# Optimization experiments

Hardware: AMD Instinct MI355X
Metric: run time of the kernel (lower is better)

Reference implementation:

```python
import math
import jax, jax.numpy as jnp
import numpy as np

H = 8
DIM = 256
HD = DIM // H
SCALE = math.sqrt(HD)
EPS = 1e-16


def _segment_softmax(scores, dst, num_nodes):
    # scores: [E, H], dst: [E] -> softmax over edges sharing the same dst
    m = jax.ops.segment_max(scores, dst, num_segments=num_nodes)  # [N, H]
    m = jnp.where(jnp.isfinite(m), m, 0.0)  # empty segments -> -inf -> 0
    e = jnp.exp(scores - m[dst])
    s = jax.ops.segment_sum(e, dst, num_segments=num_nodes)  # [N, H]
    return e / (s[dst] + EPS)


def _graph_attention(x, edges, wq, bq, wk, bk, wv, bv, wo, bo):
    # x: [N, DIM]; edges: [2, E] (src, dst). Dropout is identity (eval mode).
    N = x.shape[0]
    Q = (x @ wq + bq).reshape(N, H, HD)
    K = (x @ wk + bk).reshape(N, H, HD)
    V = (x @ wv + bv).reshape(N, H, HD)
    src, dst = edges[0], edges[1]
    scores = jnp.einsum('ehd,ehd->eh', Q[dst], K[src]) / SCALE  # [E, H]
    attn = _segment_softmax(scores, dst, N)  # [E, H]
    msgs = V[src] * attn[:, :, None]  # [E, H, HD]
    out = jax.ops.segment_sum(msgs, dst, num_segments=N).reshape(N, DIM)
    return out @ wo + bo


def _linear_params(key, fan_in, fan_out):
    k1, k2 = jax.random.split(key)
    bound = 1.0 / math.sqrt(fan_in)
    w = jax.random.uniform(k1, (fan_in, fan_out), minval=-bound, maxval=bound, dtype=jnp.float32)
    b = jax.random.uniform(k2, (fan_out,), minval=-bound, maxval=bound, dtype=jnp.float32)
    return w, b


def setup_inputs() -> dict:
    key = jax.random.key(0)
    ks = jax.random.split(key, 12)
    n_slot, n_dom = 20000, 1000
    e_slot, e_dom = 320000, 16000
    inp = {
        'slot_x': jax.random.normal(ks[0], (n_slot, DIM), dtype=jnp.float32),
        'domain_x': jax.random.normal(ks[1], (n_dom, DIM), dtype=jnp.float32),
        'slot_edges': jax.random.randint(ks[2], (2, e_slot), 0, n_slot, dtype=jnp.int32),
        'domain_edges': jax.random.randint(ks[3], (2, e_dom), 0, n_dom, dtype=jnp.int32),
    }
    names = ['wq', 'wk', 'wv', 'wo']
    for i, nm in enumerate(names):
        w, b = _linear_params(ks[4 + i], DIM, DIM)
        inp[f'slot_{nm}'] = w
        inp[f'slot_{nm}_b'] = b
    for i, nm in enumerate(names):
        w, b = _linear_params(ks[8 + i], DIM, DIM)
        inp[f'dom_{nm}'] = w
        inp[f'dom_{nm}_b'] = b
    return inp


def reference(slot_x, domain_x, slot_edges, domain_edges,
              slot_wq, slot_wq_b, slot_wk, slot_wk_b, slot_wv, slot_wv_b, slot_wo, slot_wo_b,
              dom_wq, dom_wq_b, dom_wk, dom_wk_b, dom_wv, dom_wv_b, dom_wo, dom_wo_b):
    # slot branch: self-attention on slot graph + identity residual
    slot_out = _graph_attention(slot_x, slot_edges,
                                slot_wq, slot_wq_b, slot_wk, slot_wk_b,
                                slot_wv, slot_wv_b, slot_wo, slot_wo_b) + slot_x
    # domain branch
    dom_out = _graph_attention(domain_x, domain_edges,
                               dom_wq, dom_wq_b, dom_wk, dom_wk_b,
                               dom_wv, dom_wv_b, dom_wo, dom_wo_b) + domain_x
    return slot_out, dom_out
```

## Files before the change

### kernel.cpp

```cpp
#include <hip/hip_runtime.h>
#include <hip/hip_bf16.h>

#define DIM 256
#define INV_SCALE 0.17677669529663687f
#define SM_EPS 1e-16f
#define CAP 64
#define EPT 4

typedef unsigned short ushortT;
typedef unsigned int uintT;
typedef __attribute__((ext_vector_type(8))) __bf16 bf16x8;
typedef __attribute__((ext_vector_type(4))) float f32x4;

__device__ __forceinline__ float bf2f(ushortT u) {
    return __uint_as_float(((uintT)u) << 16);
}
__device__ __forceinline__ ushortT f2bf(float f) {
    uintT u = __float_as_uint(f);
    u += 0x7FFFu + ((u >> 16) & 1u);
    return (ushortT)(u >> 16);
}
template <int CTRL>
__device__ __forceinline__ float qperm_add(float p) {
    int v = __builtin_amdgcn_update_dpp(0, __float_as_int(p), CTRL, 0xF, 0xF, true);
    return p + __int_as_float(v);
}

struct WPack { const void* w[8]; const void* b[8]; };

__device__ __forceinline__ bool sniff_m16(const ushortT* __restrict__ x) {
    int lane = threadIdx.x & 63;
    ushortT u = x[lane * 2];
    int e = (u >> 7) & 0xFF;
    bool sane = ((u & 0x7FFFu) == 0) || (e >= 0x66 && e <= 0x90);
    unsigned long long m = __ballot(sane);
    return __popcll(m) >= 32;
}

__global__ __launch_bounds__(256) void megaA(
        const void* __restrict__ xs, const void* __restrict__ xd,
        const ushortT* __restrict__ sniff_src,
        ushortT* __restrict__ xb_s, ushortT* __restrict__ xb_d,
        WPack pk, ushortT* __restrict__ wT, float* __restrict__ biasF,
        int* __restrict__ flagWs,
        const int* __restrict__ src_s, const int* __restrict__ dst_s,
        const int* __restrict__ src_d, const int* __restrict__ dst_d,
        int* __restrict__ cnt_s, int* __restrict__ cnt_d,
        int* __restrict__ col_s, int* __restrict__ col_d,
        int Es_, int Ed_, int nSc,
        int n4s, int n4d, int nA0, int nA1)
{
    const int bid = blockIdx.x;
    const int t = threadIdx.x;

    if (bid < nSc) {
        const int base = bid * (256 * EPT) + t;
        #pragma unroll
        for (int u = 0; u < EPT; ++u) {
            const int idx = base + u * 256;
            if (idx < Es_) {
                const int dv = dst_s[idx];
                const int pos = atomicAdd(&cnt_s[dv], 1);
                if (pos < CAP) col_s[(dv << 6) + pos] = src_s[idx];
            } else {
                const int e = idx - Es_;
                if (e < Ed_) {
                    const int dv = dst_d[e];
                    const int pos = atomicAdd(&cnt_d[dv], 1);
                    if (pos < CAP) col_d[(dv << 6) + pos] = src_d[e];
                }
            }
        }
        return;
    }
    const bool m16 = sniff_m16(sniff_src);
    const int li2 = bid - nSc;

    if (li2 < nA0 + nA1) {
        const bool d = li2 >= nA0;
        const int li = d ? li2 - nA0 : li2;
        const int n4 = d ? n4d : n4s;
        const int i = li * 256 + t;
        if (i >= n4) return;
        const void* x = d ? xd : xs;
        ushortT* xb = d ? xb_d : xb_s;
        if (m16) {
            ((ushort4*)xb)[i] = ((const ushort4*)x)[i];
        } else {
            float4 v = ((const float4*)x)[i];
            ushort4 o2;
            o2.x = f2bf(v.x); o2.y = f2bf(v.y); o2.z = f2bf(v.z); o2.w = f2bf(v.w);
            ((ushort4*)xb)[i] = o2;
        }
    } else if (li2 < nA0 + nA1 + 128) {
        __shared__ float sh[64][65];
        const int r0 = li2 - (nA0 + nA1);
        const int which = r0 >> 4;
        const int tile = r0 & 15;
        const int tr = tile >> 2, tc = tile & 3;
        const void* w = pk.w[which];
        const int tx = t & 63, tg = t >> 6;
        #pragma unroll
        for (int i = 0; i < 16; ++i) {
            const int r = i * 4 + tg;
            const size_t si = (size_t)(tr * 64 + r) * 256 + tc * 64 + tx;
            sh[r][tx] = m16 ? bf2f(((const ushortT*)w)[si]) : ((const float*)w)[si];
        }
        __syncthreads();
        ushortT* o = wT + (size_t)which * 65536;
        #pragma unroll
        for (int i = 0; i < 16; ++i) {
            const int r = i * 4 + tg;
            o[(size_t)(tc * 64 + r) * 256 + tr * 64 + tx] = f2bf(sh[tx][r]);
        }
    } else if (li2 < nA0 + nA1 + 136) {
        const int which = li2 - (nA0 + nA1 + 128);
        const void* b = pk.b[which];
        float v = m16 ? bf2f(((const ushortT*)b)[t]) : ((const float*)b)[t];
        biasF[which * 256 + t] = v;
    } else {
        if (t == 0) *flagWs = m16 ? 1 : 0;
    }
}

__global__ __launch_bounds__(256, 2) void megaB(
        const ushortT* __restrict__ xb_s, const ushortT* __restrict__ xb_d,
        const ushortT* __restrict__ wT, const float* __restrict__ biasF,
        ushortT* __restrict__ q_s, ushortT* __restrict__ kv_s,
        ushortT* __restrict__ q_d, ushortT* __restrict__ kv_d,
        int Ms, int Md, int nbs_, int nbq_)
{
    const int bid = blockIdx.x;
    const int by  = bid / nbq_;
    const int bx0 = bid % nbq_;
    const bool dom = bx0 >= nbs_;
    const int bx = dom ? bx0 - nbs_ : bx0;
    const ushortT* A = dom ? xb_d : xb_s;
    const int M = dom ? Md : Ms;
    const int wbase = dom ? 4 : 0;
    ushortT* Q = dom ? q_d : q_s;
    ushortT* KV = dom ? kv_d : kv_s;

    __shared__ ushortT As[64 * 256];

    const int tid  = threadIdx.x;
    const int wid  = tid >> 6;
    const int lane = tid & 63;
    const int m    = lane & 15;
    const int q    = lane >> 4;
    const int row0 = bx * 64;
    const int col0 = by * 64;
    const int colw = col0 + wid * 16 + m;

    {
        const int r  = tid >> 2;
        const int qt = tid & 3;
        const size_t rowAddr = (size_t)min(row0 + r, M - 1) * DIM;
        const int xr = r & 7;
        #pragma unroll
        for (int j = 0; j < 8; ++j) {
            const int chunk = qt * 8 + j;
            uint4 v = *(const uint4*)(A + rowAddr + chunk * 8);
            *(uint4*)&As[r * 256 + ((chunk ^ xr) * 8)] = v;
        }
    }

    const ushortT* Bp = wT + (size_t)wbase * 65536 + (size_t)colw * DIM + q * 8;
    bf16x8 bl[8][3];
    #pragma unroll
    for (int kk = 0; kk < 8; ++kk)
        #pragma unroll
        for (int z = 0; z < 3; ++z)
            bl[kk][z] = *(const bf16x8*)(Bp + (size_t)z * 65536 + kk * 32);

    f32x4 acc[3][4];
    #pragma unroll
    for (int z = 0; z < 3; ++z)
        #pragma unroll
        for (int i = 0; i < 4; ++i)
            acc[z][i] = (f32x4){0.f, 0.f, 0.f, 0.f};

    const int xm = m & 7;

    __syncthreads();

    #pragma unroll
    for (int kk = 0; kk < 8; ++kk) {
        bf16x8 af[4];
        #pragma unroll
        for (int i = 0; i < 4; ++i)
            af[i] = *(const bf16x8*)&As[(i * 16 + m) * 256 + (((q + 4 * kk) ^ xm) * 8)];
        #pragma unroll
        for (int z = 0; z < 3; ++z)
            #pragma unroll
            for (int i = 0; i < 4; ++i)
                acc[z][i] = __builtin_amdgcn_mfma_f32_16x16x32_bf16(bl[kk][z], af[i], acc[z][i], 0, 0, 0);
    }

    const int colbase = col0 + wid * 16 + q * 4;
    #pragma unroll
    for (int z = 0; z < 3; ++z) {
        const float4 b4 = *(const float4*)&biasF[(wbase + z) * 256 + colbase];
        #pragma unroll
        for (int i = 0; i < 4; ++i) {
            const int row = row0 + i * 16 + m;
            if (row < M) {
                ushort4 o;
                o.x = f2bf(acc[z][i][0] + b4.x);
                o.y = f2bf(acc[z][i][1] + b4.y);
                o.z = f2bf(acc[z][i][2] + b4.z);
                o.w = f2bf(acc[z][i][3] + b4.w);
                ushortT* C = (z == 0)
                    ? (Q + (size_t)row * DIM + colbase)
                    : (KV + (size_t)row * 512 + (z - 1) * 256 + colbase);
                *(ushort4*)C = o;
            }
        }
    }
}

__global__ __launch_bounds__(256) void attn_kernel(
        const ushortT* __restrict__ Qs, const ushortT* __restrict__ KVs,
        const int* __restrict__ cnts, const int* __restrict__ css,
        ushortT* __restrict__ aggs,
        const ushortT* __restrict__ Qd_, const ushortT* __restrict__ KVd_,
        const int* __restrict__ cntd, const int* __restrict__ csd,
        ushortT* __restrict__ aggd,
        int Ns_, int Ntot)
{
    const int g = blockIdx.x * 4 + (threadIdx.x >> 6);
    if (g >= Ntot) return;
    const bool dom = g >= Ns_;
    const int d = dom ? g - Ns_ : g;
    const int t = threadIdx.x & 63;
    const ushortT* Qb = dom ? Qd_ : Qs;
    const ushortT* KVb = dom ? KVd_ : KVs;
    const int* cnt = dom ? cntd : cnts;
    const int* colsrc = dom ? csd : css;
    ushortT* aggb = dom ? aggd : aggs;

    const uintT t4 = (uintT)t * 4;
    const size_t cbase = (size_t)d * DIM + t4;
    uint2 qv = *(const uint2*)(Qb + cbase);
    const float q0 = bf2f((ushortT)(qv.x & 0xFFFF)), q1 = bf2f((ushortT)(qv.x >> 16));
    const float q2 = bf2f((ushortT)(qv.y & 0xFFFF)), q3 = bf2f((ushortT)(qv.y >> 16));

    float a0 = 0.f, a1 = 0.f, a2 = 0.f, a3 = 0.f, den = 0.f;

    auto PROC = [&](uint2 kvc, uint2 vvc) {
        float k0 = bf2f((ushortT)(kvc.x & 0xFFFF)), k1 = bf2f((ushortT)(kvc.x >> 16));
        float k2 = bf2f((ushortT)(kvc.y & 0xFFFF)), k3 = bf2f((ushortT)(kvc.y >> 16));
        float p = q0 * k0 + q1 * k1 + q2 * k2 + q3 * k3;
        p = qperm_add<0xB1>(p);
        p = qperm_add<0x4E>(p);
        p += __shfl_xor(p, 4, 8);
        const float w = __expf(fminf(p * INV_SCALE, 60.0f));
        den += w;
        a0 += w * bf2f((ushortT)(vvc.x & 0xFFFF));
        a1 += w * bf2f((ushortT)(vvc.x >> 16));
        a2 += w * bf2f((ushortT)(vvc.y & 0xFFFF));
        a3 += w * bf2f((ushortT)(vvc.y >> 16));
    };

    int deg = cnt[d];
    if (deg > CAP) deg = CAP;
    const int* cl = colsrc + ((size_t)d << 6);
    int i = 0;
    for (; i + 8 <= deg; i += 8) {
        const int4 c0 = *(const int4*)(cl + i);
        const int4 c1 = *(const int4*)(cl + i + 4);
        const uintT o0 = ((uintT)c0.x << 9) + t4;
        const uintT o1 = ((uintT)c0.y << 9) + t4;
        const uintT o2 = ((uintT)c0.z << 9) + t4;
        const uintT o3 = ((uintT)c0.w << 9) + t4;
        const uintT o4 = ((uintT)c1.x << 9) + t4;
        const uintT o5 = ((uintT)c1.y << 9) + t4;
        const uintT o6 = ((uintT)c1.z << 9) + t4;
        const uintT o7 = ((uintT)c1.w << 9) + t4;
        uint2 k0v = *(const uint2*)(KVb + o0), v0v = *(const uint2*)(KVb + o0 + 256);
        uint2 k1v = *(const uint2*)(KVb + o1), v1v = *(const uint2*)(KVb + o1 + 256);
        uint2 k2v = *(const uint2*)(KVb + o2), v2v = *(const uint2*)(KVb + o2 + 256);
        uint2 k3v = *(const uint2*)(KVb + o3), v3v = *(const uint2*)(KVb + o3 + 256);
        uint2 k4v = *(const uint2*)(KVb + o4), v4v = *(const uint2*)(KVb + o4 + 256);
        uint2 k5v = *(const uint2*)(KVb + o5), v5v = *(const uint2*)(KVb + o5 + 256);
        uint2 k6v = *(const uint2*)(KVb + o6), v6v = *(const uint2*)(KVb + o6 + 256);
        uint2 k7v = *(const uint2*)(KVb + o7), v7v = *(const uint2*)(KVb + o7 + 256);
        PROC(k0v, v0v); PROC(k1v, v1v); PROC(k2v, v2v); PROC(k3v, v3v);
        PROC(k4v, v4v); PROC(k5v, v5v); PROC(k6v, v6v); PROC(k7v, v7v);
    }
    for (; i + 4 <= deg; i += 4) {
        const int4 c0 = *(const int4*)(cl + i);
        const uintT o0 = ((uintT)c0.x << 9) + t4;
        const uintT o1 = ((uintT)c0.y << 9) + t4;
        const uintT o2 = ((uintT)c0.z << 9) + t4;
        const uintT o3 = ((uintT)c0.w << 9) + t4;
        uint2 k0v = *(const uint2*)(KVb + o0), v0v = *(const uint2*)(KVb + o0 + 256);
        uint2 k1v = *(const uint2*)(KVb + o1), v1v = *(const uint2*)(KVb + o1 + 256);
        uint2 k2v = *(const uint2*)(KVb + o2), v2v = *(const uint2*)(KVb + o2 + 256);
        uint2 k3v = *(const uint2*)(KVb + o3), v3v = *(const uint2*)(KVb + o3 + 256);
        PROC(k0v, v0v); PROC(k1v, v1v); PROC(k2v, v2v); PROC(k3v, v3v);
    }
    for (; i < deg; ++i) {
        const uintT sb = ((uintT)cl[i] << 9) + t4;
        uint2 kv = *(const uint2*)(KVb + sb);
        uint2 vv = *(const uint2*)(KVb + sb + 256);
        PROC(kv, vv);
    }

    const float r = 1.0f / (den + SM_EPS);
    ushort4 o;
    o.x = f2bf(a0 * r); o.y = f2bf(a1 * r); o.z = f2bf(a2 * r); o.w = f2bf(a3 * r);
    *(ushort4*)(aggb + cbase) = o;
}

__global__ __launch_bounds__(256, 2) void gemm_out(
        const ushortT* __restrict__ As_, const ushortT* __restrict__ Ad_,
        const ushortT* __restrict__ wT, const float* __restrict__ biasF,
        const void* __restrict__ xs, const void* __restrict__ xd,
        void* __restrict__ dout, int Ms, int Md, int nbs,
        const int* __restrict__ flag)
{
    const bool dom = (int)blockIdx.x >= nbs;
    const int bx = dom ? blockIdx.x - nbs : blockIdx.x;
    const ushortT* A = dom ? Ad_ : As_;
    const int M = dom ? Md : Ms;
    const int widx = 3 + (dom ? 4 : 0);
    const ushortT* BT = wT + (size_t)widx * 65536;
    const float* bias = biasF + widx * 256;
    const void* res = dom ? xd : xs;
    const size_t outOff = dom ? (size_t)Ms * DIM : 0;

    __shared__ ushortT As2[64 * 256];

    const int tid  = threadIdx.x;
    const int wid  = tid >> 6;
    const int lane = tid & 63;
    const int m    = lane & 15;
    const int q    = lane >> 4;
    const int row0 = bx * 64;
    const int col0 = blockIdx.y * 64;
    const int colw = col0 + wid * 16 + m;

    {
        const int r  = tid >> 2;
        const int qt = tid & 3;
        const size_t rowAddr = (size_t)min(row0 + r, M - 1) * DIM;
        const int xr = r & 7;
        #pragma unroll
        for (int j = 0; j < 8; ++j) {
            const int chunk = qt * 8 + j;
            uint4 v = *(const uint4*)(A + rowAddr + chunk * 8);
            *(uint4*)&As2[r * 256 + ((chunk ^ xr) * 8)] = v;
        }
    }

    const ushortT* Bp = BT + (size_t)colw * DIM + q * 8;
    bf16x8 bl[8];
    #pragma unroll
    for (int kk = 0; kk < 8; ++kk)
        bl[kk] = *(const bf16x8*)(Bp + kk * 32);

    f32x4 acc[4];
    #pragma unroll
    for (int i = 0; i < 4; ++i) acc[i] = (f32x4){0.f, 0.f, 0.f, 0.f};

    const int xm = m & 7;

    __syncthreads();

    #pragma unroll
    for (int kk = 0; kk < 8; ++kk) {
        bf16x8 af[4];
        #pragma unroll
        for (int i = 0; i < 4; ++i)
            af[i] = *(const bf16x8*)&As2[(i * 16 + m) * 256 + (((q + 4 * kk) ^ xm) * 8)];
        #pragma unroll
        for (int i = 0; i < 4; ++i)
            acc[i] = __builtin_amdgcn_mfma_f32_16x16x32_bf16(bl[kk], af[i], acc[i], 0, 0, 0);
    }

    const bool m16 = (*flag != 0);
    const int colbase = col0 + wid * 16 + q * 4;
    const float4 b4 = *(const float4*)&bias[colbase];
    #pragma unroll
    for (int i = 0; i < 4; ++i) {
        const int row = row0 + i * 16 + m;
        if (row < M) {
            const size_t ridx = (size_t)row * DIM + colbase;
            float v0 = acc[i][0] + b4.x, v1 = acc[i][1] + b4.y;
            float v2 = acc[i][2] + b4.z, v3 = acc[i][3] + b4.w;
            if (m16) {
                ushort4 rv = *(const ushort4*)((const ushortT*)res + ridx);
                v0 += bf2f(rv.x); v1 += bf2f(rv.y); v2 += bf2f(rv.z); v3 += bf2f(rv.w);
                ushort4 o;
                o.x = f2bf(v0); o.y = f2bf(v1); o.z = f2bf(v2); o.w = f2bf(v3);
                *(ushort4*)((ushortT*)dout + outOff + ridx) = o;
            } else {
                float4 rv = *(const float4*)((const float*)res + ridx);
                float4 o;
                o.x = v0 + rv.x; o.y = v1 + rv.y; o.z = v2 + rv.z; o.w = v3 + rv.w;
                *(float4*)((float*)dout + outOff + ridx) = o;
            }
        }
    }
}

extern "C" void kernel_launch(void* const* d_in, const int* in_sizes, int n_in,
                              void* d_out, int out_size, void* d_ws, size_t ws_size,
                              hipStream_t stream)
{
    const void* slot_x = d_in[0];
    const void* dom_x  = d_in[1];
    const int* slot_edges = (const int*)d_in[2];
    const int* dom_edges  = (const int*)d_in[3];
    const int Ns = in_sizes[0] / DIM;
    const int Nd = in_sizes[1] / DIM;
    const int Es = in_sizes[2] / 2;
    const int Ed = in_sizes[3] / 2;

    WPack pk;
    for (int i = 0; i < 8; ++i) { pk.w[i] = d_in[4 + 2 * i]; pk.b[i] = d_in[5 + 2 * i]; }

    char* p = (char*)d_ws;
    size_t o = 0;
    auto take = [&](size_t b) { void* r = p + o; o = (o + b + 255) & ~(size_t)255; return r; };
    const size_t ndS = (size_t)Ns * DIM;
    const size_t ndD = (size_t)Nd * DIM;
    ushortT* xb_s  = (ushortT*)take(ndS * 2);
    ushortT* q_s   = (ushortT*)take(ndS * 2);
    ushortT* kv_s  = (ushortT*)take(2 * ndS * 2);
    ushortT* agg_s = (ushortT*)take(ndS * 2);
    ushortT* xb_d  = (ushortT*)take(ndD * 2);
    ushortT* q_d   = (ushortT*)take(ndD * 2);
    ushortT* kv_d  = (ushortT*)take(2 * ndD * 2);
    ushortT* agg_d = (ushortT*)take(ndD * 2);
    ushortT* wT    = (ushortT*)take(8 * 65536 * 2);
    float*   biasF = (float*)take(8 * 256 * 4);
    int* cnt_s = (int*)take((size_t)(Ns + Nd) * 4);
    int* cnt_d = cnt_s + Ns;
    int* col_s = (int*)take((size_t)Ns * CAP * 4);
    int* col_d = (int*)take((size_t)Nd * CAP * 4);
    int* flagWs = (int*)take(256);

    const int* src_s = slot_edges;
    const int* dst_s = slot_edges + Es;
    const int* src_d = dom_edges;
    const int* dst_d = dom_edges + Ed;

    const int n4s = Ns * DIM / 4, n4d = Nd * DIM / 4;
    const int nbs = (Ns + 63) / 64;
    const int nbd = (Nd + 63) / 64;
    const int nbq = nbs + nbd;

    (void)hipMemsetAsync(cnt_s, 0, (size_t)(Ns + Nd) * 4, stream);

    const int Etot = Es + Ed;
    const int nSc = (Etot + 256 * EPT - 1) / (256 * EPT);
    const int nA0 = (n4s + 255) / 256;
    const int nA1 = (n4d + 255) / 256;
    hipLaunchKernelGGL(megaA, dim3(nSc + nA0 + nA1 + 136 + 1), dim3(256), 0, stream,
                       slot_x, dom_x, (const ushortT*)slot_x, xb_s, xb_d,
                       pk, wT, biasF, flagWs,
                       src_s, dst_s, src_d, dst_d,
                       cnt_s, cnt_d, col_s, col_d,
                       Es, Ed, nSc, n4s, n4d, nA0, nA1);

    hipLaunchKernelGGL(megaB, dim3(nbq * 4), dim3(256), 0, stream,
                       xb_s, xb_d, wT, biasF, q_s, kv_s, q_d, kv_d,
                       Ns, Nd, nbs, nbq);

    const int Ntot = Ns + Nd;
    hipLaunchKernelGGL(attn_kernel, dim3((Ntot + 3) / 4), dim3(256), 0, stream,
                       q_s, kv_s, cnt_s, col_s, agg_s,
                       q_d, kv_d, cnt_d, col_d, agg_d,
                       Ns, Ntot);

    hipLaunchKernelGGL(gemm_out, dim3(nbq, DIM / 64), dim3(256), 0, stream,
                       agg_s, agg_d, wT, biasF, slot_x, dom_x, d_out,
                       Ns, Nd, nbs, flagWs);
}
```

Before: 225.7 us.

## Fuse attention with output GEMM via tile counters; move edge scatter into QKV GEMM

Merges the attention-aggregation kernel and the output projection GEMM into one launch. Attention blocks bump a per-tile counter, and GEMM blocks in the same group spin-wait on that counter before consuming the tile, so the two phases overlap. The edge CSR scatter moves from the conversion kernel into the QKV GEMM launch, and the QKV GEMM epilogue now stages its output through shared memory for wider coalesced stores. The spin-wait assumes the producer blocks are scheduled before or alongside their consumers, which carries deadlock and occupancy risk, and the added shared buffers raise LDS use.

```diff
diff --git a/kernel.cpp b/kernel.cpp
--- a/kernel.cpp
+++ b/kernel.cpp
@@ -6,6 +6,7 @@
 #define SM_EPS 1e-16f
 #define CAP 64
 #define EPT 4
+#define GRP 20
 
 typedef unsigned short ushortT;
 typedef unsigned int uintT;
@@ -43,18 +44,74 @@
         ushortT* __restrict__ xb_s, ushortT* __restrict__ xb_d,
         WPack pk, ushortT* __restrict__ wT, float* __restrict__ biasF,
         int* __restrict__ flagWs,
+        int n4s, int n4d, int nA0, int nA1)
+{
+    const bool m16 = sniff_m16(sniff_src);
+    const int bid = blockIdx.x;
+    const int t = threadIdx.x;
+
+    if (bid < nA0 + nA1) {
+        const bool d = bid >= nA0;
+        const int li = d ? bid - nA0 : bid;
+        const int n4 = d ? n4d : n4s;
+        const int i = li * 256 + t;
+        if (i >= n4) return;
+        const void* x = d ? xd : xs;
+        ushortT* xb = d ? xb_d : xb_s;
+        if (m16) {
+            ((ushort4*)xb)[i] = ((const ushort4*)x)[i];
+        } else {
+            float4 v = ((const float4*)x)[i];
+            ushort4 o2;
+            o2.x = f2bf(v.x); o2.y = f2bf(v.y); o2.z = f2bf(v.z); o2.w = f2bf(v.w);
+            ((ushort4*)xb)[i] = o2;
+        }
+    } else if (bid < nA0 + nA1 + 128) {
+        __shared__ float sh[64][65];
+        const int r0 = bid - (nA0 + nA1);
+        const int which = r0 >> 4;
+        const int tile = r0 & 15;
+        const int tr = tile >> 2, tc = tile & 3;
+        const void* w = pk.w[which];
+        const int tx = t & 63, tg = t >> 6;
+        #pragma unroll
+        for (int i = 0; i < 16; ++i) {
+            const int r = i * 4 + tg;
+            const size_t si = (size_t)(tr * 64 + r) * 256 + tc * 64 + tx;
+            sh[r][tx] = m16 ? bf2f(((const ushortT*)w)[si]) : ((const float*)w)[si];
+        }
+        __syncthreads();
+        ushortT* o = wT + (size_t)which * 65536;
+        #pragma unroll
+        for (int i = 0; i < 16; ++i) {
+            const int r = i * 4 + tg;
+            o[(size_t)(tc * 64 + r) * 256 + tr * 64 + tx] = f2bf(sh[tx][r]);
+        }
+    } else if (bid < nA0 + nA1 + 136) {
+        const int which = bid - (nA0 + nA1 + 128);
+        const void* b = pk.b[which];
+        float v = m16 ? bf2f(((const ushortT*)b)[t]) : ((const float*)b)[t];
+        biasF[which * 256 + t] = v;
+    } else {
+        if (t == 0) *flagWs = m16 ? 1 : 0;
+    }
+}
+
+__global__ __launch_bounds__(256, 2) void megaB(
+        const ushortT* __restrict__ xb_s, const ushortT* __restrict__ xb_d,
+        const ushortT* __restrict__ wT, const float* __restrict__ biasF,
+        ushortT* __restrict__ q_s, ushortT* __restrict__ kv_s,
+        ushortT* __restrict__ q_d, ushortT* __restrict__ kv_d,
+        int Ms, int Md, int nbs_, int nbq_, int nSc,
         const int* __restrict__ src_s, const int* __restrict__ dst_s,
         const int* __restrict__ src_d, const int* __restrict__ dst_d,
         int* __restrict__ cnt_s, int* __restrict__ cnt_d,
         int* __restrict__ col_s, int* __restrict__ col_d,
-        int Es_, int Ed_, int nSc,
-        int n4s, int n4d, int nA0, int nA1)
+        int Es_, int Ed_)
 {
     const int bid = blockIdx.x;
-    const int t = threadIdx.x;
-
     if (bid < nSc) {
-        const int base = bid * (256 * EPT) + t;
+        const int base = bid * (256 * EPT) + threadIdx.x;
         #pragma unroll
         for (int u = 0; u < EPT; ++u) {
             const int idx = base + u * 256;
@@ -73,66 +130,9 @@
         }
         return;
     }
-    const bool m16 = sniff_m16(sniff_src);
-    const int li2 = bid - nSc;
-
-    if (li2 < nA0 + nA1) {
-        const bool d = li2 >= nA0;
-        const int li = d ? li2 - nA0 : li2;
-        const int n4 = d ? n4d : n4s;
-        const int i = li * 256 + t;
-        if (i >= n4) return;
-        const void* x = d ? xd : xs;
-        ushortT* xb = d ? xb_d : xb_s;
-        if (m16) {
-            ((ushort4*)xb)[i] = ((const ushort4*)x)[i];
-        } else {
-            float4 v = ((const float4*)x)[i];
-            ushort4 o2;
-            o2.x = f2bf(v.x); o2.y = f2bf(v.y); o2.z = f2bf(v.z); o2.w = f2bf(v.w);
-            ((ushort4*)xb)[i] = o2;
-        }
-    } else if (li2 < nA0 + nA1 + 128) {
-        __shared__ float sh[64][65];
-        const int r0 = li2 - (nA0 + nA1);
-        const int which = r0 >> 4;
-        const int tile = r0 & 15;
-        const int tr = tile >> 2, tc = tile & 3;
-        const void* w = pk.w[which];
-        const int tx = t & 63, tg = t >> 6;
-        #pragma unroll
-        for (int i = 0; i < 16; ++i) {
-            const int r = i * 4 + tg;
-            const size_t si = (size_t)(tr * 64 + r) * 256 + tc * 64 + tx;
-            sh[r][tx] = m16 ? bf2f(((const ushortT*)w)[si]) : ((const float*)w)[si];
-        }
-        __syncthreads();
-        ushortT* o = wT + (size_t)which * 65536;
-        #pragma unroll
-        for (int i = 0; i < 16; ++i) {
-            const int r = i * 4 + tg;
-            o[(size_t)(tc * 64 + r) * 256 + tr * 64 + tx] = f2bf(sh[tx][r]);
-        }
-    } else if (li2 < nA0 + nA1 + 136) {
-        const int which = li2 - (nA0 + nA1 + 128);
-        const void* b = pk.b[which];
-        float v = m16 ? bf2f(((const ushortT*)b)[t]) : ((const float*)b)[t];
-        biasF[which * 256 + t] = v;
-    } else {
-        if (t == 0) *flagWs = m16 ? 1 : 0;
-    }
-}
-
-__global__ __launch_bounds__(256, 2) void megaB(
-        const ushortT* __restrict__ xb_s, const ushortT* __restrict__ xb_d,
-        const ushortT* __restrict__ wT, const float* __restrict__ biasF,
-        ushortT* __restrict__ q_s, ushortT* __restrict__ kv_s,
-        ushortT* __restrict__ q_d, ushortT* __restrict__ kv_d,
-        int Ms, int Md, int nbs_, int nbq_)
-{
-    const int bid = blockIdx.x;
-    const int by  = bid / nbq_;
-    const int bx0 = bid % nbq_;
+    const int gbid = bid - nSc;
+    const int by  = gbid / nbq_;
+    const int bx0 = gbid % nbq_;
     const bool dom = bx0 >= nbs_;
     const int bx = dom ? bx0 - nbs_ : bx0;
     const ushortT* A = dom ? xb_d : xb_s;
@@ -142,6 +142,7 @@
     ushortT* KV = dom ? kv_d : kv_s;
 
     __shared__ ushortT As[64 * 256];
+    __shared__ ushortT Cs[3][64 * 70];
 
     const int tid  = threadIdx.x;
     const int wid  = tid >> 6;
@@ -197,148 +198,185 @@
                 acc[z][i] = __builtin_amdgcn_mfma_f32_16x16x32_bf16(bl[kk][z], af[i], acc[z][i], 0, 0, 0);
     }
 
-    const int colbase = col0 + wid * 16 + q * 4;
     #pragma unroll
     for (int z = 0; z < 3; ++z) {
-        const float4 b4 = *(const float4*)&biasF[(wbase + z) * 256 + colbase];
+        const float4 b4 = *(const float4*)&biasF[(wbase + z) * 256 + col0 + wid * 16 + q * 4];
         #pragma unroll
         for (int i = 0; i < 4; ++i) {
-            const int row = row0 + i * 16 + m;
-            if (row < M) {
-                ushort4 o;
-                o.x = f2bf(acc[z][i][0] + b4.x);
-                o.y = f2bf(acc[z][i][1] + b4.y);
-                o.z = f2bf(acc[z][i][2] + b4.z);
-                o.w = f2bf(acc[z][i][3] + b4.w);
+            const int r = i * 16 + m;
+            ushort4 o;
+            o.x = f2bf(acc[z][i][0] + b4.x);
+            o.y = f2bf(acc[z][i][1] + b4.y);
+            o.z = f2bf(acc[z][i][2] + b4.z);
+            o.w = f2bf(acc[z][i][3] + b4.w);
+            *(ushort4*)&Cs[z][r * 70 + wid * 16 + q * 4] = o;
+        }
+    }
+    __syncthreads();
+
+    {
+        const int r = tid >> 2;
+        const int c = (tid & 3) * 16;
+        const int row = row0 + r;
+        if (row < M) {
+            #pragma unroll
+            for (int z = 0; z < 3; ++z) {
+                uint4 v0 = *(const uint4*)&Cs[z][r * 70 + c];
+                uint4 v1 = *(const uint4*)&Cs[z][r * 70 + c + 8];
                 ushortT* C = (z == 0)
-                    ? (Q + (size_t)row * DIM + colbase)
-                    : (KV + (size_t)row * 512 + (z - 1) * 256 + colbase);
-                *(ushort4*)C = o;
+                    ? (Q + (size_t)row * DIM + col0 + c)
+                    : (KV + (size_t)row * 512 + (z - 1) * 256 + col0 + c);
+                *(uint4*)C = v0;
+                *(uint4*)(C + 8) = v1;
             }
         }
     }
 }
 
-__global__ __launch_bounds__(256) void attn_kernel(
+__global__ __launch_bounds__(256, 4) void fusedK(
         const ushortT* __restrict__ Qs, const ushortT* __restrict__ KVs,
         const int* __restrict__ cnts, const int* __restrict__ css,
         ushortT* __restrict__ aggs,
         const ushortT* __restrict__ Qd_, const ushortT* __restrict__ KVd_,
         const int* __restrict__ cntd, const int* __restrict__ csd,
         ushortT* __restrict__ aggd,
-        int Ns_, int Ntot)
-{
-    const int g = blockIdx.x * 4 + (threadIdx.x >> 6);
-    if (g >= Ntot) return;
-    const bool dom = g >= Ns_;
-    const int d = dom ? g - Ns_ : g;
-    const int t = threadIdx.x & 63;
-    const ushortT* Qb = dom ? Qd_ : Qs;
-    const ushortT* KVb = dom ? KVd_ : KVs;
-    const int* cnt = dom ? cntd : cnts;
-    const int* colsrc = dom ? csd : css;
-    ushortT* aggb = dom ? aggd : aggs;
-
-    const uintT t4 = (uintT)t * 4;
-    const size_t cbase = (size_t)d * DIM + t4;
-    uint2 qv = *(const uint2*)(Qb + cbase);
-    const float q0 = bf2f((ushortT)(qv.x & 0xFFFF)), q1 = bf2f((ushortT)(qv.x >> 16));
-    const float q2 = bf2f((ushortT)(qv.y & 0xFFFF)), q3 = bf2f((ushortT)(qv.y >> 16));
-
-    float a0 = 0.f, a1 = 0.f, a2 = 0.f, a3 = 0.f, den = 0.f;
-
-    auto PROC = [&](uint2 kvc, uint2 vvc) {
-        float k0 = bf2f((ushortT)(kvc.x & 0xFFFF)), k1 = bf2f((ushortT)(kvc.x >> 16));
-        float k2 = bf2f((ushortT)(kvc.y & 0xFFFF)), k3 = bf2f((ushortT)(kvc.y >> 16));
-        float p = q0 * k0 + q1 * k1 + q2 * k2 + q3 * k3;
-        p = qperm_add<0xB1>(p);
-        p = qperm_add<0x4E>(p);
-        p += __shfl_xor(p, 4, 8);
-        const float w = __expf(fminf(p * INV_SCALE, 60.0f));
-        den += w;
-        a0 += w * bf2f((ushortT)(vvc.x & 0xFFFF));
-        a1 += w * bf2f((ushortT)(vvc.x >> 16));
-        a2 += w * bf2f((ushortT)(vvc.y & 0xFFFF));
-        a3 += w * bf2f((ushortT)(vvc.y >> 16));
-    };
-
-    int deg = cnt[d];
-    if (deg > CAP) deg = CAP;
-    const int* cl = colsrc + ((size_t)d << 6);
-    int i = 0;
-    for (; i + 8 <= deg; i += 8) {
-        const int4 c0 = *(const int4*)(cl + i);
-        const int4 c1 = *(const int4*)(cl + i + 4);
-        const uintT o0 = ((uintT)c0.x << 9) + t4;
-        const uintT o1 = ((uintT)c0.y << 9) + t4;
-        const uintT o2 = ((uintT)c0.z << 9) + t4;
-        const uintT o3 = ((uintT)c0.w << 9) + t4;
-        const uintT o4 = ((uintT)c1.x << 9) + t4;
-        const uintT o5 = ((uintT)c1.y << 9) + t4;
-        const uintT o6 = ((uintT)c1.z << 9) + t4;
-        const uintT o7 = ((uintT)c1.w << 9) + t4;
-        uint2 k0v = *(const uint2*)(KVb + o0), v0v = *(const uint2*)(KVb + o0 + 256);
-        uint2 k1v = *(const uint2*)(KVb + o1), v1v = *(const uint2*)(KVb + o1 + 256);
-        uint2 k2v = *(const uint2*)(KVb + o2), v2v = *(const uint2*)(KVb + o2 + 256);
-        uint2 k3v = *(const uint2*)(KVb + o3), v3v = *(const uint2*)(KVb + o3 + 256);
-        uint2 k4v = *(const uint2*)(KVb + o4), v4v = *(const uint2*)(KVb + o4 + 256);
-        uint2 k5v = *(const uint2*)(KVb + o5), v5v = *(const uint2*)(KVb + o5 + 256);
-        uint2 k6v = *(const uint2*)(KVb + o6), v6v = *(const uint2*)(KVb + o6 + 256);
-        uint2 k7v = *(const uint2*)(KVb + o7), v7v = *(const uint2*)(KVb + o7 + 256);
-        PROC(k0v, v0v); PROC(k1v, v1v); PROC(k2v, v2v); PROC(k3v, v3v);
-        PROC(k4v, v4v); PROC(k5v, v5v); PROC(k6v, v6v); PROC(k7v, v7v);
-    }
-    for (; i + 4 <= deg; i += 4) {
-        const int4 c0 = *(const int4*)(cl + i);
-        const uintT o0 = ((uintT)c0.x << 9) + t4;
-        const uintT o1 = ((uintT)c0.y << 9) + t4;
-        const uintT o2 = ((uintT)c0.z << 9) + t4;
-        const uintT o3 = ((uintT)c0.w << 9) + t4;
-        uint2 k0v = *(const uint2*)(KVb + o0), v0v = *(const uint2*)(KVb + o0 + 256);
-        uint2 k1v = *(const uint2*)(KVb + o1), v1v = *(const uint2*)(KVb + o1 + 256);
-        uint2 k2v = *(const uint2*)(KVb + o2), v2v = *(const uint2*)(KVb + o2 + 256);
-        uint2 k3v = *(const uint2*)(KVb + o3), v3v = *(const uint2*)(KVb + o3 + 256);
-        PROC(k0v, v0v); PROC(k1v, v1v); PROC(k2v, v2v); PROC(k3v, v3v);
-    }
-    for (; i < deg; ++i) {
-        const uintT sb = ((uintT)cl[i] << 9) + t4;
-        uint2 kv = *(const uint2*)(KVb + sb);
-        uint2 vv = *(const uint2*)(KVb + sb + 256);
-        PROC(kv, vv);
-    }
-
-    const float r = 1.0f / (den + SM_EPS);
-    ushort4 o;
-    o.x = f2bf(a0 * r); o.y = f2bf(a1 * r); o.z = f2bf(a2 * r); o.w = f2bf(a3 * r);
-    *(ushort4*)(aggb + cbase) = o;
-}
-
-__global__ __launch_bounds__(256, 2) void gemm_out(
-        const ushortT* __restrict__ As_, const ushortT* __restrict__ Ad_,
         const ushortT* __restrict__ wT, const float* __restrict__ biasF,
         const void* __restrict__ xs, const void* __restrict__ xd,
-        void* __restrict__ dout, int Ms, int Md, int nbs,
-        const int* __restrict__ flag)
+        void* __restrict__ dout, int* __restrict__ tileDone,
+        const int* __restrict__ flag,
+        int Ns_, int Nd_, int Ntot, int nbs, int nbq, int nUnits)
 {
-    const bool dom = (int)blockIdx.x >= nbs;
-    const int bx = dom ? blockIdx.x - nbs : blockIdx.x;
-    const ushortT* A = dom ? Ad_ : As_;
-    const int M = dom ? Md : Ms;
+    const int grp = blockIdx.x / GRP;
+    const int pos = blockIdx.x % GRP;
+    const int tid = threadIdx.x;
+
+    if (pos < 16) {
+        const int u = grp * 16 + pos;
+        if (u >= nUnits) return;
+        const int g = u * 4 + (tid >> 6);
+        if (g < Ntot) {
+            const bool dom = g >= Ns_;
+            const int d = dom ? g - Ns_ : g;
+            const int t = tid & 63;
+            const ushortT* Qb = dom ? Qd_ : Qs;
+            const ushortT* KVb = dom ? KVd_ : KVs;
+            const int* cnt = dom ? cntd : cnts;
+            const int* colsrc = dom ? csd : css;
+            ushortT* aggb = dom ? aggd : aggs;
+
+            const uintT t4 = (uintT)t * 4;
+            const size_t cbase = (size_t)d * DIM + t4;
+            uint2 qv = *(const uint2*)(Qb + cbase);
+            const float q0 = bf2f((ushortT)(qv.x & 0xFFFF)), q1 = bf2f((ushortT)(qv.x >> 16));
+            const float q2 = bf2f((ushortT)(qv.y & 0xFFFF)), q3 = bf2f((ushortT)(qv.y >> 16));
+
+            float a0 = 0.f, a1 = 0.f, a2 = 0.f, a3 = 0.f, den = 0.f;
+
+            auto PROC = [&](uint2 kvc, uint2 vvc) {
+                float k0 = bf2f((ushortT)(kvc.x & 0xFFFF)), k1 = bf2f((ushortT)(kvc.x >> 16));
+                float k2 = bf2f((ushortT)(kvc.y & 0xFFFF)), k3 = bf2f((ushortT)(kvc.y >> 16));
+                float p = q0 * k0 + q1 * k1 + q2 * k2 + q3 * k3;
+                p = qperm_add<0xB1>(p);
+                p = qperm_add<0x4E>(p);
+                p += __shfl_xor(p, 4, 8);
+                const float w = __expf(fminf(p * INV_SCALE, 60.0f));
+                den += w;
+                a0 += w * bf2f((ushortT)(vvc.x & 0xFFFF));
+                a1 += w * bf2f((ushortT)(vvc.x >> 16));
+                a2 += w * bf2f((ushortT)(vvc.y & 0xFFFF));
+                a3 += w * bf2f((ushortT)(vvc.y >> 16));
+            };
+
+            int deg = cnt[d];
+            if (deg > CAP) deg = CAP;
+            const int* cl = colsrc + ((size_t)d << 6);
+            int i = 0;
+            for (; i + 8 <= deg; i += 8) {
+                const int4 c0 = *(const int4*)(cl + i);
+                const int4 c1 = *(const int4*)(cl + i + 4);
+                const uintT o0 = ((uintT)c0.x << 9) + t4;
+                const uintT o1 = ((uintT)c0.y << 9) + t4;
+                const uintT o2 = ((uintT)c0.z << 9) + t4;
+                const uintT o3 = ((uintT)c0.w << 9) + t4;
+                const uintT o4 = ((uintT)c1.x << 9) + t4;
+                const uintT o5 = ((uintT)c1.y << 9) + t4;
+                const uintT o6 = ((uintT)c1.z << 9) + t4;
+                const uintT o7 = ((uintT)c1.w << 9) + t4;
+                uint2 k0v = *(const uint2*)(KVb + o0), v0v = *(const uint2*)(KVb + o0 + 256);
+                uint2 k1v = *(const uint2*)(KVb + o1), v1v = *(const uint2*)(KVb + o1 + 256);
+                uint2 k2v = *(const uint2*)(KVb + o2), v2v = *(const uint2*)(KVb + o2 + 256);
+                uint2 k3v = *(const uint2*)(KVb + o3), v3v = *(const uint2*)(KVb + o3 + 256);
+                uint2 k4v = *(const uint2*)(KVb + o4), v4v = *(const uint2*)(KVb + o4 + 256);
+                uint2 k5v = *(const uint2*)(KVb + o5), v5v = *(const uint2*)(KVb + o5 + 256);
+                uint2 k6v = *(const uint2*)(KVb + o6), v6v = *(const uint2*)(KVb + o6 + 256);
+                uint2 k7v = *(const uint2*)(KVb + o7), v7v = *(const uint2*)(KVb + o7 + 256);
+                PROC(k0v, v0v); PROC(k1v, v1v); PROC(k2v, v2v); PROC(k3v, v3v);
+                PROC(k4v, v4v); PROC(k5v, v5v); PROC(k6v, v6v); PROC(k7v, v7v);
+            }
+            for (; i + 4 <= deg; i += 4) {
+                const int4 c0 = *(const int4*)(cl + i);
+                const uintT o0 = ((uintT)c0.x << 9) + t4;
+                const uintT o1 = ((uintT)c0.y << 9) + t4;
+                const uintT o2 = ((uintT)c0.z << 9) + t4;
+                const uintT o3 = ((uintT)c0.w << 9) + t4;
+                uint2 k0v = *(const uint2*)(KVb + o0), v0v = *(const uint2*)(KVb + o0 + 256);
+                uint2 k1v = *(const uint2*)(KVb + o1), v1v = *(const uint2*)(KVb + o1 + 256);
+                uint2 k2v = *(const uint2*)(KVb + o2), v2v = *(const uint2*)(KVb + o2 + 256);
+                uint2 k3v = *(const uint2*)(KVb + o3), v3v = *(const uint2*)(KVb + o3 + 256);
+                PROC(k0v, v0v); PROC(k1v, v1v); PROC(k2v, v2v); PROC(k3v, v3v);
+            }
+            for (; i < deg; ++i) {
+                const uintT sb = ((uintT)cl[i] << 9) + t4;
+                uint2 kv = *(const uint2*)(KVb + sb);
+                uint2 vv = *(const uint2*)(KVb + sb + 256);
+                PROC(kv, vv);
+            }
+
+            const float r = 1.0f / (den + SM_EPS);
+            ushort4 o;
+            o.x = f2bf(a0 * r); o.y = f2bf(a1 * r); o.z = f2bf(a2 * r); o.w = f2bf(a3 * r);
+            *(ushort4*)(aggb + cbase) = o;
+        }
+        __syncthreads();
+        if (tid == 0) {
+            const int g0 = u * 4;
+            const int tile = (g0 < Ns_) ? (g0 >> 6) : (nbs + ((g0 - Ns_) >> 6));
+            __hip_atomic_fetch_add(&tileDone[tile], 1, __ATOMIC_RELEASE,
+                                   __HIP_MEMORY_SCOPE_AGENT);
+        }
+        return;
+    }
+
+    const int tile = grp;
+    if (tile >= nbq) return;
+    const bool dom = tile >= nbs;
+    const int bx = dom ? tile - nbs : tile;
+    const int M = dom ? Nd_ : Ns_;
+    const int row0 = bx * 64;
+    const int rows = min(64, M - row0);
+    const int target = (rows + 3) >> 2;
+
+    const ushortT* A = dom ? aggd : aggs;
     const int widx = 3 + (dom ? 4 : 0);
     const ushortT* BT = wT + (size_t)widx * 65536;
     const float* bias = biasF + widx * 256;
     const void* res = dom ? xd : xs;
-    const size_t outOff = dom ? (size_t)Ms * DIM : 0;
+    const size_t outOff = dom ? (size_t)Ns_ * DIM : 0;
+    const int col0 = (pos - 16) * 64;
 
     __shared__ ushortT As2[64 * 256];
 
-    const int tid  = threadIdx.x;
+    if (tid == 0) {
+        while (__hip_atomic_load(&tileDone[tile], __ATOMIC_ACQUIRE,
+                                 __HIP_MEMORY_SCOPE_AGENT) < target)
+            __builtin_amdgcn_s_sleep(8);
+    }
+    __syncthreads();
+
     const int wid  = tid >> 6;
     const int lane = tid & 63;
     const int m    = lane & 15;
     const int q    = lane >> 4;
-    const int row0 = bx * 64;
-    const int col0 = blockIdx.y * 64;
     const int colw = col0 + wid * 16 + m;
 
     {
@@ -421,6 +459,10 @@
     WPack pk;
     for (int i = 0; i < 8; ++i) { pk.w[i] = d_in[4 + 2 * i]; pk.b[i] = d_in[5 + 2 * i]; }
 
+    const int nbs = (Ns + 63) / 64;
+    const int nbd = (Nd + 63) / 64;
+    const int nbq = nbs + nbd;
+
     char* p = (char*)d_ws;
     size_t o = 0;
     auto take = [&](size_t b) { void* r = p + o; o = (o + b + 255) & ~(size_t)255; return r; };
@@ -436,8 +478,9 @@
     ushortT* agg_d = (ushortT*)take(ndD * 2);
     ushortT* wT    = (ushortT*)take(8 * 65536 * 2);
     float*   biasF = (float*)take(8 * 256 * 4);
-    int* cnt_s = (int*)take((size_t)(Ns + Nd) * 4);
+    int* cnt_s = (int*)take((size_t)(Ns + Nd + nbq) * 4);
     int* cnt_d = cnt_s + Ns;
+    int* tileDone = cnt_d + Nd;
     int* col_s = (int*)take((size_t)Ns * CAP * 4);
     int* col_d = (int*)take((size_t)Nd * CAP * 4);
     int* flagWs = (int*)take(256);
@@ -448,34 +491,28 @@
     const int* dst_d = dom_edges + Ed;
 
     const int n4s = Ns * DIM / 4, n4d = Nd * DIM / 4;
-    const int nbs = (Ns + 63) / 64;
-    const int nbd = (Nd + 63) / 64;
-    const int nbq = nbs + nbd;
-
-    (void)hipMemsetAsync(cnt_s, 0, (size_t)(Ns + Nd) * 4, stream);
+
+    (void)hipMemsetAsync(cnt_s, 0, (size_t)(Ns + Nd + nbq) * 4, stream);
+
+    const int nA0 = (n4s + 255) / 256;
+    const int nA1 = (n4d + 255) / 256;
+    hipLaunchKernelGGL(megaA, dim3(nA0 + nA1 + 136 + 1), dim3(256), 0, stream,
+                       slot_x, dom_x, (const ushortT*)slot_x, xb_s, xb_d,
+                       pk, wT, biasF, flagWs, n4s, n4d, nA0, nA1);
 
     const int Etot = Es + Ed;
     const int nSc = (Etot + 256 * EPT - 1) / (256 * EPT);
-    const int nA0 = (n4s + 255) / 256;
-    const int nA1 = (n4d + 255) / 256;
-    hipLaunchKernelGGL(megaA, dim3(nSc + nA0 + nA1 + 136 + 1), dim3(256), 0, stream,
-                       slot_x, dom_x, (const ushortT*)slot_x, xb_s, xb_d,
-                       pk, wT, biasF, flagWs,
+    hipLaunchKernelGGL(megaB, dim3(nSc + nbq * 4), dim3(256), 0, stream,
+                       xb_s, xb_d, wT, biasF, q_s, kv_s, q_d, kv_d,
+                       Ns, Nd, nbs, nbq, nSc,
                        src_s, dst_s, src_d, dst_d,
-                       cnt_s, cnt_d, col_s, col_d,
-                       Es, Ed, nSc, n4s, n4d, nA0, nA1);
-
-    hipLaunchKernelGGL(megaB, dim3(nbq * 4), dim3(256), 0, stream,
-                       xb_s, xb_d, wT, biasF, q_s, kv_s, q_d, kv_d,
-                       Ns, Nd, nbs, nbq);
+                       cnt_s, cnt_d, col_s, col_d, Es, Ed);
 
     const int Ntot = Ns + Nd;
-    hipLaunchKernelGGL(attn_kernel, dim3((Ntot + 3) / 4), dim3(256), 0, stream,
+    const int nUnits = (Ntot + 3) / 4;
+    hipLaunchKernelGGL(fusedK, dim3(nbq * GRP), dim3(256), 0, stream,
                        q_s, kv_s, cnt_s, col_s, agg_s,
                        q_d, kv_d, cnt_d, col_d, agg_d,
-                       Ns, Ntot);
-
-    hipLaunchKernelGGL(gemm_out, dim3(nbq, DIM / 64), dim3(256), 0, stream,
-                       agg_s, agg_d, wT, biasF, slot_x, dom_x, d_out,
-                       Ns, Nd, nbs, flagWs);
-}
+                       wT, biasF, slot_x, dom_x, d_out, tileDone, flagWs,
+                       Ns, Nd, Ntot, nbs, nbq, nUnits);
+}
```

New measurement: 613.0 us. 2.72x slower.
